# Optimization experiments

Measured on AMD Instinct MI355X. Metric: run time of the kernel, lower is better.

## Reference

```python
import jax, jax.numpy as jnp
import numpy as np

N_NODES = 200000
N_EDGES = 3200000
NUM_GRAPHS = 100
WIN = 30
H1, H2, OUT = 500, 20, 4


def setup_inputs() -> dict:
    key = jax.random.key(0)
    ks = jax.random.split(key, 8)
    features = jax.random.normal(ks[0], (N_NODES, WIN), dtype=jnp.float32)
    src = jax.random.randint(ks[1], (N_EDGES,), 0, N_NODES, dtype=jnp.int32)
    dst = jax.random.randint(ks[2], (N_EDGES,), 0, N_NODES, dtype=jnp.int32)
    # contiguous equal-size graphs: 2000 nodes per graph -> ids sorted 0..99
    graph_ids = (jnp.arange(N_NODES, dtype=jnp.int32) // (N_NODES // NUM_GRAPHS))
    W1 = jax.random.normal(ks[3], (WIN, H1), dtype=jnp.float32) / np.sqrt(WIN)
    b1 = jnp.zeros((H1,), jnp.float32)
    W2 = jax.random.normal(ks[4], (H1, H2), dtype=jnp.float32) / np.sqrt(H1)
    b2 = jnp.zeros((H2,), jnp.float32)
    W3 = jax.random.normal(ks[5], (H2, OUT), dtype=jnp.float32) / np.sqrt(H2)
    b3 = jnp.zeros((OUT,), jnp.float32)
    return {"features": features, "src": src, "dst": dst, "graph_ids": graph_ids,
            "num_graphs": NUM_GRAPHS, "W1": W1, "b1": b1, "W2": W2, "b2": b2,
            "W3": W3, "b3": b3}


def reference(features, src, dst, graph_ids, num_graphs, W1, b1, W2, b2, W3, b3):
    N = features.shape[0]
    ones = jnp.ones(src.shape[0], dtype=features.dtype)
    # DGL GraphConv norm='both': D_out^{-1/2} on src side, D_in^{-1/2} on dst side
    deg_out = jnp.maximum(jax.ops.segment_sum(ones, src, num_segments=N), 1.0)
    deg_in = jnp.maximum(jax.ops.segment_sum(ones, dst, num_segments=N), 1.0)
    x = features * jax.lax.rsqrt(deg_out)[:, None]
    # aggregate first (in_feats < out_feats), then dense transform
    agg = jax.ops.segment_sum(x[src], dst, num_segments=N)          # [N, 30]
    agg = agg * jax.lax.rsqrt(deg_in)[:, None]
    h = jax.nn.silu(agg @ W1 + b1)                                   # [N, 500]
    pooled = jax.ops.segment_max(h, graph_ids, num_segments=num_graphs)  # [G, 500]
    y = jax.nn.silu(pooled @ W2 + b2)                                # dropout = identity (eval)
    return jax.nn.sigmoid(y @ W3 + b3)                               # [G, 4]
```

## Files before the change

kernel.cpp:

```cpp
#include <hip/hip_runtime.h>
#include <hip/hip_fp16.h>

#define WIN 30
#define H1 500
#define H1P 512
#define H2 20
#define OUTD 4
#define CS 4
#define NBIN 49152
#define NBINW (NBIN/4)
#define NCH 48
#define RPB 512
#define MAXPB 9216
#define BINCHUNK 8192
#define NBMAX 400

typedef _Float16 f16x8 __attribute__((ext_vector_type(8)));
typedef float f32x4 __attribute__((ext_vector_type(4)));

__global__ __launch_bounds__(512) void k_hist(const int* __restrict__ src,
                                              unsigned* __restrict__ partial,
                                              int E) {
    __shared__ unsigned h[NBINW];
    const int tid = threadIdx.x;
    const int r = blockIdx.x / NCH, c = blockIdx.x % NCH;
    const int base = r * NBIN;
    for (int j = tid; j < NBINW; j += 512) h[j] = 0;
    __syncthreads();
    const int ce = ((E + NCH - 1) / NCH + 3) & ~3;
    const int start = c * ce;
    const int end = min(E, start + ce);
    for (int i = start + tid * 4; i < end; i += 512 * 4) {
        if (i + 3 < end) {
            int4 s4 = *(const int4*)(src + i);
            unsigned d;
            d = (unsigned)(s4.x - base); if (d < NBIN) atomicAdd(&h[d >> 2], 1u << ((d & 3) * 8));
            d = (unsigned)(s4.y - base); if (d < NBIN) atomicAdd(&h[d >> 2], 1u << ((d & 3) * 8));
            d = (unsigned)(s4.z - base); if (d < NBIN) atomicAdd(&h[d >> 2], 1u << ((d & 3) * 8));
            d = (unsigned)(s4.w - base); if (d < NBIN) atomicAdd(&h[d >> 2], 1u << ((d & 3) * 8));
        } else {
            for (int k = i; k < end; ++k) {
                unsigned d = (unsigned)(src[k] - base);
                if (d < NBIN) atomicAdd(&h[d >> 2], 1u << ((d & 3) * 8));
            }
        }
    }
    __syncthreads();
    unsigned* outp = partial + (size_t)blockIdx.x * NBINW;
    for (int j = tid; j < NBINW; j += 512) outp[j] = h[j];
}

__global__ __launch_bounds__(256) void k_merge(const unsigned* __restrict__ partial,
                                               int* __restrict__ degO, int N, int nr) {
    int w = blockIdx.x * 256 + threadIdx.x;
    if (w >= nr * NBINW) return;
    int r = w / NBINW, lw = w - r * NBINW;
    const unsigned* p = partial + (size_t)(r * NCH) * NBINW + lw;
    unsigned b0 = 0, b1 = 0, b2 = 0, b3 = 0;
    for (int c = 0; c < NCH; ++c) {
        unsigned v = p[(size_t)c * NBINW];
        b0 += v & 0xFFu; b1 += (v >> 8) & 0xFFu;
        b2 += (v >> 16) & 0xFFu; b3 += v >> 24;
    }
    int n0 = r * NBIN + 4 * lw;
    if (n0 + 3 < N) {
        *(int4*)(degO + n0) = make_int4((int)b0, (int)b1, (int)b2, (int)b3);
    } else if (n0 < N) {
        degO[n0] = (int)b0;
        if (n0 + 1 < N) degO[n0 + 1] = (int)b1;
        if (n0 + 2 < N) degO[n0 + 2] = (int)b2;
    }
}

__global__ __launch_bounds__(256) void k_prep(const float* __restrict__ feat,
                                              const int* __restrict__ degO,
                                              __half* __restrict__ xh, int N32) {
    int i = blockIdx.x * 256 + threadIdx.x;
    if (i < N32) {
        int n = i >> 5, d = i & 31;
        float v = 0.f;
        if (d < WIN) v = feat[(size_t)n * WIN + d] * rsqrtf((float)max(degO[n], 1));
        xh[i] = __float2half(v);
    }
}

__global__ __launch_bounds__(256) void k_w1prep(const float* __restrict__ W1,
                                                __half* __restrict__ w1cm) {
    int i = blockIdx.x * 256 + threadIdx.x;
    int c = i >> 5, k = i & 31;
    float v = (k < WIN && c < H1) ? W1[k * H1 + c] : 0.f;
    w1cm[i] = __float2half(v);
}

__global__ __launch_bounds__(1024) void k_bin(const int* __restrict__ src,
                                              const int* __restrict__ dst,
                                              int* __restrict__ gcur,
                                              unsigned* __restrict__ ebuf,
                                              int E, int NB) {
    __shared__ int cnt[NBMAX];
    __shared__ int base[NBMAX];
    const int tid = threadIdx.x;
    for (int j = tid; j < NB; j += 1024) cnt[j] = 0;
    __syncthreads();
    const int start = blockIdx.x * BINCHUNK;
    const int end = min(E, start + BINCHUNK);
    for (int i = start + tid; i < end; i += 1024)
        atomicAdd(&cnt[dst[i] >> 9], 1);
    __syncthreads();
    for (int j = tid; j < NB; j += 1024) {
        int c = cnt[j];
        base[j] = j * MAXPB + (c ? atomicAdd(&gcur[j], c) : 0);
        cnt[j] = 0;
    }
    __syncthreads();
    for (int i = start + tid; i < end; i += 1024) {
        int d = dst[i];
        int b = d >> 9;
        int idx = atomicAdd(&cnt[b], 1);
        int pos = base[b] + idx;
        if (pos < (b + 1) * MAXPB)
            ebuf[pos] = ((unsigned)src[i] << 9) | (unsigned)(d & 511);
    }
}

__global__ __launch_bounds__(1024) void k_agg(const __half* __restrict__ xh,
                                              const unsigned* __restrict__ ebuf,
                                              const int* __restrict__ gcur,
                                              __half* __restrict__ agg, int N) {
    __shared__ unsigned es[MAXPB];
    __shared__ int cnt[RPB + 1];
    __shared__ int cur[RPB];
    const int tid = threadIdx.x;
    const int b = blockIdx.x;
    for (int j = tid; j < RPB; j += 1024) { cnt[j + 1] = 0; cur[j] = 0; }
    if (tid == 0) cnt[0] = 0;
    __syncthreads();
    const int ne = min(gcur[b], MAXPB);
    const unsigned* eb = ebuf + (size_t)b * MAXPB;
    for (int i = tid; i < ne; i += 1024)
        atomicAdd(&cnt[(int)(eb[i] & (RPB - 1)) + 1], 1);
    __syncthreads();
    if (tid < 64) {
        const int i0 = tid * 8;
        int s[8];
        int run = 0;
#pragma unroll
        for (int k = 0; k < 8; ++k) { run += cnt[i0 + k + 1]; s[k] = run; }
        int inc = run;
#pragma unroll
        for (int o = 1; o < 64; o <<= 1) {
            int u = __shfl_up(inc, o, 64);
            if (tid >= o) inc += u;
        }
        const int ex = inc - run;
#pragma unroll
        for (int k = 0; k < 8; ++k) cnt[i0 + k + 1] = ex + s[k];
    }
    __syncthreads();
    for (int i = tid; i < ne; i += 1024) {
        unsigned p = eb[i];
        int ld = (int)(p & (RPB - 1));
        int idx = atomicAdd(&cur[ld], 1);
        es[cnt[ld] + idx] = p;
    }
    __syncthreads();
    for (int task = tid; task < RPB * 4; task += 1024) {
        const int node_l = task >> 2;
        const int c8 = (task & 3) * 8;
        const int o0 = cnt[node_l], o1 = cnt[node_l + 1];
        float a0 = 0.f, a1 = 0.f, a2 = 0.f, a3 = 0.f;
        float a4 = 0.f, a5 = 0.f, a6 = 0.f, a7 = 0.f;
        int j = o0;
#pragma unroll 2
        for (; j + 1 < o1; j += 2) {
            unsigned p0 = es[j], p1 = es[j + 1];
            union { uint4 u4; __half2 h2[4]; } x0, x1;
            x0.u4 = *(const uint4*)(xh + (size_t)(p0 >> 9) * 32 + c8);
            x1.u4 = *(const uint4*)(xh + (size_t)(p1 >> 9) * 32 + c8);
            a0 += __low2float(x0.h2[0]) + __low2float(x1.h2[0]);
            a1 += __high2float(x0.h2[0]) + __high2float(x1.h2[0]);
            a2 += __low2float(x0.h2[1]) + __low2float(x1.h2[1]);
            a3 += __high2float(x0.h2[1]) + __high2float(x1.h2[1]);
            a4 += __low2float(x0.h2[2]) + __low2float(x1.h2[2]);
            a5 += __high2float(x0.h2[2]) + __high2float(x1.h2[2]);
            a6 += __low2float(x0.h2[3]) + __low2float(x1.h2[3]);
            a7 += __high2float(x0.h2[3]) + __high2float(x1.h2[3]);
        }
        if (j < o1) {
            unsigned p0 = es[j];
            union { uint4 u4; __half2 h2[4]; } x0;
            x0.u4 = *(const uint4*)(xh + (size_t)(p0 >> 9) * 32 + c8);
            a0 += __low2float(x0.h2[0]);  a1 += __high2float(x0.h2[0]);
            a2 += __low2float(x0.h2[1]);  a3 += __high2float(x0.h2[1]);
            a4 += __low2float(x0.h2[2]);  a5 += __high2float(x0.h2[2]);
            a6 += __low2float(x0.h2[3]);  a7 += __high2float(x0.h2[3]);
        }
        const int node = b * RPB + node_l;
        if (node < N) {
            float deg = (float)(o1 - o0);
            float r = rsqrtf(fmaxf(deg, 1.f));
            union { uint4 u4; __half2 h2[4]; } y;
            y.h2[0] = __floats2half2_rn(a0 * r, a1 * r);
            y.h2[1] = __floats2half2_rn(a2 * r, a3 * r);
            y.h2[2] = __floats2half2_rn(a4 * r, a5 * r);
            y.h2[3] = __floats2half2_rn(a6 * r, a7 * r);
            *(uint4*)(agg + (size_t)node * 32 + c8) = y.u4;
        }
    }
}

__global__ __launch_bounds__(256) void k_gemm(const __half* __restrict__ agg,
                                              const __half* __restrict__ w1cm,
                                              const float* __restrict__ b1,
                                              float* __restrict__ pooled,
                                              int NPG, int G) {
    const int bid = blockIdx.x;
    const int g = bid / CS, c = bid % CS;
    const int tid = threadIdx.x;
    const int w = tid >> 6;
    const int l = tid & 63;
    const int lo = l & 15, hi = l >> 4;

    f16x8 bfr[8];
#pragma unroll
    for (int ct = 0; ct < 8; ++ct) {
        int col = c * 128 + ct * 16 + lo;
        bfr[ct] = *(const f16x8*)(w1cm + (size_t)col * 32 + hi * 8);
    }
    float vmax[8], vmin[8];
#pragma unroll
    for (int ct = 0; ct < 8; ++ct) { vmax[ct] = -INFINITY; vmin[ct] = INFINITY; }

    const int mts = NPG >> 4;
    for (int mt = w; mt < mts; mt += 4) {
        int node = g * NPG + mt * 16 + lo;
        f16x8 a = *(const f16x8*)(agg + (size_t)node * 32 + hi * 8);
#pragma unroll
        for (int ct = 0; ct < 8; ++ct) {
            f32x4 acc = {0.f, 0.f, 0.f, 0.f};
            acc = __builtin_amdgcn_mfma_f32_16x16x32_f16(a, bfr[ct], acc, 0, 0, 0);
#pragma unroll
            for (int q = 0; q < 4; ++q) {
                vmax[ct] = fmaxf(vmax[ct], acc[q]);
                vmin[ct] = fminf(vmin[ct], acc[q]);
            }
        }
    }
#pragma unroll
    for (int ct = 0; ct < 8; ++ct) {
        vmax[ct] = fmaxf(vmax[ct], __shfl_xor(vmax[ct], 16, 64));
        vmax[ct] = fmaxf(vmax[ct], __shfl_xor(vmax[ct], 32, 64));
        vmin[ct] = fminf(vmin[ct], __shfl_xor(vmin[ct], 16, 64));
        vmin[ct] = fminf(vmin[ct], __shfl_xor(vmin[ct], 32, 64));
    }
    __shared__ float red[2][4][8][16];
    if (hi == 0) {
#pragma unroll
        for (int ct = 0; ct < 8; ++ct) {
            red[0][w][ct][lo] = vmax[ct];
            red[1][w][ct][lo] = vmin[ct];
        }
    }
    __syncthreads();
    if (tid < 128) {
        int ct = tid >> 4, col16 = tid & 15;
        float m = fmaxf(fmaxf(red[0][0][ct][col16], red[0][1][ct][col16]),
                        fmaxf(red[0][2][ct][col16], red[0][3][ct][col16]));
        float n = fminf(fminf(red[1][0][ct][col16], red[1][1][ct][col16]),
                        fminf(red[1][2][ct][col16], red[1][3][ct][col16]));
        int col = c * 128 + ct * 16 + col16;
        float bb = (col < H1) ? b1[col] : 0.f;
        m += bb; n += bb;
        float sm = m / (1.f + __expf(-m));
        float sn = n / (1.f + __expf(-n));
        pooled[(size_t)g * H1P + col] = fmaxf(sm, sn);
    }
}

__global__ __launch_bounds__(64) void k_head(const float* __restrict__ pooled,
                                             const float* __restrict__ W2,
                                             const float* __restrict__ b2,
                                             const float* __restrict__ W3,
                                             const float* __restrict__ b3,
                                             float* __restrict__ out, int G) {
    const int g = blockIdx.x;
    const int t = threadIdx.x;
    __shared__ float y[H2];
    if (t < H2) {
        float acc = b2[t];
        for (int k = 0; k < H1; ++k)
            acc = fmaf(pooled[(size_t)g * H1P + k], W2[k * H2 + t], acc);
        y[t] = acc / (1.f + __expf(-acc));
    }
    __syncthreads();
    if (t < OUTD) {
        float acc = b3[t];
#pragma unroll
        for (int k = 0; k < H2; ++k) acc = fmaf(y[k], W3[k * OUTD + t], acc);
        out[g * OUTD + t] = 1.f / (1.f + __expf(-acc));
    }
}

static inline size_t align256(size_t x) { return (x + 255) & ~(size_t)255; }

extern "C" void kernel_launch(void* const* d_in, const int* in_sizes, int n_in,
                              void* d_out, int out_size, void* d_ws, size_t ws_size,
                              hipStream_t stream) {
    const float* feat = (const float*)d_in[0];
    const int*   src  = (const int*)d_in[1];
    const int*   dst  = (const int*)d_in[2];
    const float* W1 = (const float*)d_in[5];
    const float* b1 = (const float*)d_in[6];
    const float* W2 = (const float*)d_in[7];
    const float* b2 = (const float*)d_in[8];
    const float* W3 = (const float*)d_in[9];
    const float* b3 = (const float*)d_in[10];
    float* out = (float*)d_out;

    const int N = in_sizes[0] / WIN;
    const int E = in_sizes[1];
    const int G = out_size / OUTD;
    const int NPG = N / G;
    const int nr = (N + NBIN - 1) / NBIN;
    const int NB = (N + RPB - 1) / RPB;

    char* ws = (char*)d_ws;
    size_t off = 0;
    int*      degO    = (int*)(ws + off);      off += align256((size_t)N * 4);
    unsigned* partial = (unsigned*)(ws + off); off += align256((size_t)nr * NCH * NBINW * 4);
    __half*   xh      = (__half*)(ws + off);   off += align256((size_t)N * 32 * 2);
    __half*   w1cm    = (__half*)(ws + off);   off += align256((size_t)H1P * 32 * 2);
    float*    pooled  = (float*)(ws + off);    off += align256((size_t)G * H1P * 4);
    __half*   agg     = (__half*)(ws + off);   off += align256((size_t)N * 32 * 2);
    int*      gcur    = (int*)(ws + off);      off += align256((size_t)NB * 4);
    unsigned* ebuf    = (unsigned*)(ws + off); off += align256((size_t)NB * MAXPB * 4 + 256);
    (void)ws_size; (void)n_in;

    hipMemsetAsync(gcur, 0, (size_t)NB * 4, stream);

    k_hist<<<nr * NCH, 512, 0, stream>>>(src, partial, E);
    k_merge<<<(nr * NBINW + 255) / 256, 256, 0, stream>>>(partial, degO, N, nr);
    k_w1prep<<<(H1P * 32) / 256, 256, 0, stream>>>(W1, w1cm);
    k_prep<<<(N * 32 + 255) / 256, 256, 0, stream>>>(feat, degO, xh, N * 32);

    k_bin<<<(E + BINCHUNK - 1) / BINCHUNK, 1024, 0, stream>>>(src, dst, gcur, ebuf, E, NB);
    k_agg<<<NB, 1024, 0, stream>>>(xh, ebuf, gcur, agg, N);

    k_gemm<<<G * CS, 256, 0, stream>>>(agg, w1cm, b1, pooled, NPG, G);
    k_head<<<G, 64, 0, stream>>>(pooled, W2, b2, W3, b3, out, G);
}
```

Before: 165.8 us.

## Fuse aggregation with W1 MFMA and per-block min/max pooling

The aggregation kernel now keeps each block's aggregated rows in shared memory and runs the W1 MFMA on them directly. It reduces per-column max/min into shared memory through order-preserving uint atomics, then writes per-block partial results. A new kernel merges the partials per graph, applies bias, SiLU and the head, so the agg round trip through global memory and the separate GEMM launch go away. Block size is halved (256 rows, 512 threads) to fit shared memory and raise block count, at the cost of shared atomics and at most two graph slots per block.

```diff
diff --git a/kernel.cpp b/kernel.cpp
--- a/kernel.cpp
+++ b/kernel.cpp
@@ -6,17 +6,25 @@
 #define H1P 512
 #define H2 20
 #define OUTD 4
-#define CS 4
 #define NBIN 49152
 #define NBINW (NBIN/4)
 #define NCH 48
-#define RPB 512
-#define MAXPB 9216
+#define RPB 256
+#define MAXPB 4608
 #define BINCHUNK 8192
-#define NBMAX 400
+#define NBMAX 800
 
 typedef _Float16 f16x8 __attribute__((ext_vector_type(8)));
 typedef float f32x4 __attribute__((ext_vector_type(4)));
+
+__device__ __forceinline__ unsigned enc_f32(float f) {
+    unsigned b = __float_as_uint(f);
+    return b ^ ((unsigned)((int)b >> 31) | 0x80000000u);
+}
+__device__ __forceinline__ float dec_f32(unsigned u) {
+    unsigned b = (u & 0x80000000u) ? (u ^ 0x80000000u) : ~u;
+    return __uint_as_float(b);
+}
 
 __global__ __launch_bounds__(512) void k_hist(const int* __restrict__ src,
                                               unsigned* __restrict__ partial,
@@ -105,7 +113,7 @@
     const int start = blockIdx.x * BINCHUNK;
     const int end = min(E, start + BINCHUNK);
     for (int i = start + tid; i < end; i += 1024)
-        atomicAdd(&cnt[dst[i] >> 9], 1);
+        atomicAdd(&cnt[dst[i] >> 8], 1);
     __syncthreads();
     for (int j = tid; j < NB; j += 1024) {
         int c = cnt[j];
@@ -115,37 +123,45 @@
     __syncthreads();
     for (int i = start + tid; i < end; i += 1024) {
         int d = dst[i];
-        int b = d >> 9;
+        int b = d >> 8;
         int idx = atomicAdd(&cnt[b], 1);
         int pos = base[b] + idx;
         if (pos < (b + 1) * MAXPB)
-            ebuf[pos] = ((unsigned)src[i] << 9) | (unsigned)(d & 511);
-    }
-}
-
-__global__ __launch_bounds__(1024) void k_agg(const __half* __restrict__ xh,
-                                              const unsigned* __restrict__ ebuf,
-                                              const int* __restrict__ gcur,
-                                              __half* __restrict__ agg, int N) {
+            ebuf[pos] = ((unsigned)src[i] << 8) | (unsigned)(d & 255);
+    }
+}
+
+__global__ __launch_bounds__(512) void k_agg(const __half* __restrict__ xh,
+                                             const unsigned* __restrict__ ebuf,
+                                             const int* __restrict__ gcur,
+                                             const __half* __restrict__ w1cm,
+                                             unsigned* __restrict__ bmm,
+                                             int N, int NPG) {
     __shared__ unsigned es[MAXPB];
     __shared__ int cnt[RPB + 1];
     __shared__ int cur[RPB];
+    __shared__ __half xtile[RPB * 40];
+    __shared__ unsigned mmenc[2 * H1P * 2];
     const int tid = threadIdx.x;
     const int b = blockIdx.x;
-    for (int j = tid; j < RPB; j += 1024) { cnt[j + 1] = 0; cur[j] = 0; }
+    for (int j = tid; j < RPB; j += 512) { cnt[j + 1] = 0; cur[j] = 0; }
     if (tid == 0) cnt[0] = 0;
+    for (int j = tid; j < H1P * 2; j += 512) {
+        mmenc[2 * j + 0] = 0u;
+        mmenc[2 * j + 1] = 0xFFFFFFFFu;
+    }
     __syncthreads();
     const int ne = min(gcur[b], MAXPB);
     const unsigned* eb = ebuf + (size_t)b * MAXPB;
-    for (int i = tid; i < ne; i += 1024)
+    for (int i = tid; i < ne; i += 512)
         atomicAdd(&cnt[(int)(eb[i] & (RPB - 1)) + 1], 1);
     __syncthreads();
     if (tid < 64) {
-        const int i0 = tid * 8;
-        int s[8];
+        const int i0 = tid * 4;
+        int s[4];
         int run = 0;
 #pragma unroll
-        for (int k = 0; k < 8; ++k) { run += cnt[i0 + k + 1]; s[k] = run; }
+        for (int k = 0; k < 4; ++k) { run += cnt[i0 + k + 1]; s[k] = run; }
         int inc = run;
 #pragma unroll
         for (int o = 1; o < 64; o <<= 1) {
@@ -154,17 +170,17 @@
         }
         const int ex = inc - run;
 #pragma unroll
-        for (int k = 0; k < 8; ++k) cnt[i0 + k + 1] = ex + s[k];
-    }
-    __syncthreads();
-    for (int i = tid; i < ne; i += 1024) {
+        for (int k = 0; k < 4; ++k) cnt[i0 + k + 1] = ex + s[k];
+    }
+    __syncthreads();
+    for (int i = tid; i < ne; i += 512) {
         unsigned p = eb[i];
         int ld = (int)(p & (RPB - 1));
         int idx = atomicAdd(&cur[ld], 1);
         es[cnt[ld] + idx] = p;
     }
     __syncthreads();
-    for (int task = tid; task < RPB * 4; task += 1024) {
+    for (int task = tid; task < RPB * 4; task += 512) {
         const int node_l = task >> 2;
         const int c8 = (task & 3) * 8;
         const int o0 = cnt[node_l], o1 = cnt[node_l + 1];
@@ -175,8 +191,8 @@
         for (; j + 1 < o1; j += 2) {
             unsigned p0 = es[j], p1 = es[j + 1];
             union { uint4 u4; __half2 h2[4]; } x0, x1;
-            x0.u4 = *(const uint4*)(xh + (size_t)(p0 >> 9) * 32 + c8);
-            x1.u4 = *(const uint4*)(xh + (size_t)(p1 >> 9) * 32 + c8);
+            x0.u4 = *(const uint4*)(xh + (size_t)(p0 >> 8) * 32 + c8);
+            x1.u4 = *(const uint4*)(xh + (size_t)(p1 >> 8) * 32 + c8);
             a0 += __low2float(x0.h2[0]) + __low2float(x1.h2[0]);
             a1 += __high2float(x0.h2[0]) + __high2float(x1.h2[0]);
             a2 += __low2float(x0.h2[1]) + __low2float(x1.h2[1]);
@@ -189,107 +205,95 @@
         if (j < o1) {
             unsigned p0 = es[j];
             union { uint4 u4; __half2 h2[4]; } x0;
-            x0.u4 = *(const uint4*)(xh + (size_t)(p0 >> 9) * 32 + c8);
+            x0.u4 = *(const uint4*)(xh + (size_t)(p0 >> 8) * 32 + c8);
             a0 += __low2float(x0.h2[0]);  a1 += __high2float(x0.h2[0]);
             a2 += __low2float(x0.h2[1]);  a3 += __high2float(x0.h2[1]);
             a4 += __low2float(x0.h2[2]);  a5 += __high2float(x0.h2[2]);
             a6 += __low2float(x0.h2[3]);  a7 += __high2float(x0.h2[3]);
         }
-        const int node = b * RPB + node_l;
-        if (node < N) {
-            float deg = (float)(o1 - o0);
-            float r = rsqrtf(fmaxf(deg, 1.f));
-            union { uint4 u4; __half2 h2[4]; } y;
-            y.h2[0] = __floats2half2_rn(a0 * r, a1 * r);
-            y.h2[1] = __floats2half2_rn(a2 * r, a3 * r);
-            y.h2[2] = __floats2half2_rn(a4 * r, a5 * r);
-            y.h2[3] = __floats2half2_rn(a6 * r, a7 * r);
-            *(uint4*)(agg + (size_t)node * 32 + c8) = y.u4;
-        }
-    }
-}
-
-__global__ __launch_bounds__(256) void k_gemm(const __half* __restrict__ agg,
-                                              const __half* __restrict__ w1cm,
-                                              const float* __restrict__ b1,
-                                              float* __restrict__ pooled,
-                                              int NPG, int G) {
-    const int bid = blockIdx.x;
-    const int g = bid / CS, c = bid % CS;
-    const int tid = threadIdx.x;
-    const int w = tid >> 6;
-    const int l = tid & 63;
-    const int lo = l & 15, hi = l >> 4;
-
-    f16x8 bfr[8];
-#pragma unroll
-    for (int ct = 0; ct < 8; ++ct) {
-        int col = c * 128 + ct * 16 + lo;
-        bfr[ct] = *(const f16x8*)(w1cm + (size_t)col * 32 + hi * 8);
-    }
-    float vmax[8], vmin[8];
-#pragma unroll
-    for (int ct = 0; ct < 8; ++ct) { vmax[ct] = -INFINITY; vmin[ct] = INFINITY; }
-
-    const int mts = NPG >> 4;
-    for (int mt = w; mt < mts; mt += 4) {
-        int node = g * NPG + mt * 16 + lo;
-        f16x8 a = *(const f16x8*)(agg + (size_t)node * 32 + hi * 8);
-#pragma unroll
-        for (int ct = 0; ct < 8; ++ct) {
-            f32x4 acc = {0.f, 0.f, 0.f, 0.f};
-            acc = __builtin_amdgcn_mfma_f32_16x16x32_f16(a, bfr[ct], acc, 0, 0, 0);
-#pragma unroll
-            for (int q = 0; q < 4; ++q) {
-                vmax[ct] = fmaxf(vmax[ct], acc[q]);
-                vmin[ct] = fminf(vmin[ct], acc[q]);
+        float deg = (float)(o1 - o0);
+        float r = rsqrtf(fmaxf(deg, 1.f));
+        union { uint4 u4; __half2 h2[4]; } y;
+        y.h2[0] = __floats2half2_rn(a0 * r, a1 * r);
+        y.h2[1] = __floats2half2_rn(a2 * r, a3 * r);
+        y.h2[2] = __floats2half2_rn(a4 * r, a5 * r);
+        y.h2[3] = __floats2half2_rn(a6 * r, a7 * r);
+        *(uint4*)(&xtile[node_l * 40 + c8]) = y.u4;
+    }
+    __syncthreads();
+    {
+        const int wv = tid >> 6;
+        const int l = tid & 63;
+        const int lo = l & 15, hi = l >> 4;
+        const int bbase = b * RPB;
+        const int g0 = bbase / NPG;
+        f16x8 bfr[4];
+#pragma unroll
+        for (int j = 0; j < 4; ++j) {
+            int col = (wv * 4 + j) * 16 + lo;
+            bfr[j] = *(const f16x8*)(w1cm + (size_t)col * 32 + hi * 8);
+        }
+        for (int mt = 0; mt < RPB / 16; ++mt) {
+            if (bbase + mt * 16 >= N) break;
+            f16x8 a = *(const f16x8*)(&xtile[(mt * 16 + lo) * 40 + hi * 8]);
+            int slot = (bbase + mt * 16) / NPG - g0;
+#pragma unroll
+            for (int j = 0; j < 4; ++j) {
+                f32x4 acc = {0.f, 0.f, 0.f, 0.f};
+                acc = __builtin_amdgcn_mfma_f32_16x16x32_f16(a, bfr[j], acc, 0, 0, 0);
+                float mx = fmaxf(fmaxf(acc[0], acc[1]), fmaxf(acc[2], acc[3]));
+                float mn = fminf(fminf(acc[0], acc[1]), fminf(acc[2], acc[3]));
+                mx = fmaxf(mx, __shfl_xor(mx, 16, 64));
+                mx = fmaxf(mx, __shfl_xor(mx, 32, 64));
+                mn = fminf(mn, __shfl_xor(mn, 16, 64));
+                mn = fminf(mn, __shfl_xor(mn, 32, 64));
+                if (hi == 0) {
+                    int col = (wv * 4 + j) * 16 + lo;
+                    atomicMax(&mmenc[(slot * H1P + col) * 2 + 0], enc_f32(mx));
+                    atomicMin(&mmenc[(slot * H1P + col) * 2 + 1], enc_f32(mn));
+                }
             }
         }
     }
-#pragma unroll
-    for (int ct = 0; ct < 8; ++ct) {
-        vmax[ct] = fmaxf(vmax[ct], __shfl_xor(vmax[ct], 16, 64));
-        vmax[ct] = fmaxf(vmax[ct], __shfl_xor(vmax[ct], 32, 64));
-        vmin[ct] = fminf(vmin[ct], __shfl_xor(vmin[ct], 16, 64));
-        vmin[ct] = fminf(vmin[ct], __shfl_xor(vmin[ct], 32, 64));
-    }
-    __shared__ float red[2][4][8][16];
-    if (hi == 0) {
-#pragma unroll
-        for (int ct = 0; ct < 8; ++ct) {
-            red[0][w][ct][lo] = vmax[ct];
-            red[1][w][ct][lo] = vmin[ct];
-        }
-    }
-    __syncthreads();
-    if (tid < 128) {
-        int ct = tid >> 4, col16 = tid & 15;
-        float m = fmaxf(fmaxf(red[0][0][ct][col16], red[0][1][ct][col16]),
-                        fmaxf(red[0][2][ct][col16], red[0][3][ct][col16]));
-        float n = fminf(fminf(red[1][0][ct][col16], red[1][1][ct][col16]),
-                        fminf(red[1][2][ct][col16], red[1][3][ct][col16]));
-        int col = c * 128 + ct * 16 + col16;
-        float bb = (col < H1) ? b1[col] : 0.f;
-        m += bb; n += bb;
-        float sm = m / (1.f + __expf(-m));
-        float sn = n / (1.f + __expf(-n));
-        pooled[(size_t)g * H1P + col] = fmaxf(sm, sn);
-    }
-}
-
-__global__ __launch_bounds__(64) void k_head(const float* __restrict__ pooled,
-                                             const float* __restrict__ W2,
-                                             const float* __restrict__ b2,
-                                             const float* __restrict__ W3,
-                                             const float* __restrict__ b3,
-                                             float* __restrict__ out, int G) {
+    __syncthreads();
+    for (int j = tid; j < 2 * H1P * 2; j += 512)
+        bmm[(size_t)b * (2 * H1P * 2) + j] = mmenc[j];
+}
+
+__global__ __launch_bounds__(512) void k_rh(const unsigned* __restrict__ bmm,
+                                            const float* __restrict__ b1,
+                                            const float* __restrict__ W2,
+                                            const float* __restrict__ b2,
+                                            const float* __restrict__ W3,
+                                            const float* __restrict__ b3,
+                                            float* __restrict__ out,
+                                            int NPG, int NB) {
     const int g = blockIdx.x;
     const int t = threadIdx.x;
+    __shared__ float ph[H1P];
     __shared__ float y[H2];
+    unsigned me = 0u, mn = 0xFFFFFFFFu;
+    const int bFirst = (g * NPG) / RPB;
+    const int bLast = (g * NPG + NPG - 1) / RPB;
+    for (int b = bFirst; b <= bLast; ++b) {
+        int slot = g - (b * RPB) / NPG;
+        if (slot >= 0 && slot < 2) {
+            const unsigned* p = bmm + (size_t)b * (2 * H1P * 2) + ((size_t)slot * H1P + t) * 2;
+            me = max(me, p[0]);
+            mn = min(mn, p[1]);
+        }
+    }
+    float m = dec_f32(me), n = dec_f32(mn);
+    float bb = (t < H1) ? b1[t] : 0.f;
+    m += bb; n += bb;
+    float sm = m / (1.f + __expf(-m));
+    float sn = n / (1.f + __expf(-n));
+    ph[t] = fmaxf(sm, sn);
+    __syncthreads();
     if (t < H2) {
         float acc = b2[t];
         for (int k = 0; k < H1; ++k)
-            acc = fmaf(pooled[(size_t)g * H1P + k], W2[k * H2 + t], acc);
+            acc = fmaf(ph[k], W2[k * H2 + t], acc);
         y[t] = acc / (1.f + __expf(-acc));
     }
     __syncthreads();
@@ -330,10 +334,9 @@
     unsigned* partial = (unsigned*)(ws + off); off += align256((size_t)nr * NCH * NBINW * 4);
     __half*   xh      = (__half*)(ws + off);   off += align256((size_t)N * 32 * 2);
     __half*   w1cm    = (__half*)(ws + off);   off += align256((size_t)H1P * 32 * 2);
-    float*    pooled  = (float*)(ws + off);    off += align256((size_t)G * H1P * 4);
-    __half*   agg     = (__half*)(ws + off);   off += align256((size_t)N * 32 * 2);
     int*      gcur    = (int*)(ws + off);      off += align256((size_t)NB * 4);
     unsigned* ebuf    = (unsigned*)(ws + off); off += align256((size_t)NB * MAXPB * 4 + 256);
+    unsigned* bmm     = (unsigned*)(ws + off); off += align256((size_t)NB * 2 * H1P * 2 * 4);
     (void)ws_size; (void)n_in;
 
     hipMemsetAsync(gcur, 0, (size_t)NB * 4, stream);
@@ -344,8 +347,7 @@
     k_prep<<<(N * 32 + 255) / 256, 256, 0, stream>>>(feat, degO, xh, N * 32);
 
     k_bin<<<(E + BINCHUNK - 1) / BINCHUNK, 1024, 0, stream>>>(src, dst, gcur, ebuf, E, NB);
-    k_agg<<<NB, 1024, 0, stream>>>(xh, ebuf, gcur, agg, N);
-
-    k_gemm<<<G * CS, 256, 0, stream>>>(agg, w1cm, b1, pooled, NPG, G);
-    k_head<<<G, 64, 0, stream>>>(pooled, W2, b2, W3, b3, out, G);
-}
+    k_agg<<<NB, 512, 0, stream>>>(xh, ebuf, gcur, w1cm, bmm, N, NPG);
+
+    k_rh<<<G, 512, 0, stream>>>(bmm, b1, W2, b2, W3, b3, out, NPG, NB);
+}
```

Result: slower. 181.0 us (+9.2%).

## Fuse prep kernels, merge GEMM with head, drop memset, widen agg unroll

Applied to the files above, without the earlier changes.

Folds the degree merge, feature scaling and W1 conversion into one prep kernel. Fuses the per-graph GEMM/max-pool with the MLP head into one 512-thread block per graph. The gcur memset moves into the histogram kernel, and NBIN grows so nr drops from 5 to 4. The aggregation loop is unrolled by four. Together these cut launch count and intermediate traffic, but the fused GEMM now runs only 100 blocks with no split across column chunks, so parallelism drops.

```diff
diff --git a/kernel.cpp b/kernel.cpp
--- a/kernel.cpp
+++ b/kernel.cpp
@@ -6,8 +6,7 @@
 #define H1P 512
 #define H2 20
 #define OUTD 4
-#define CS 4
-#define NBIN 49152
+#define NBIN 61440
 #define NBINW (NBIN/4)
 #define NCH 48
 #define RPB 512
@@ -20,9 +19,12 @@
 
 __global__ __launch_bounds__(512) void k_hist(const int* __restrict__ src,
                                               unsigned* __restrict__ partial,
-                                              int E) {
+                                              int* __restrict__ gcur,
+                                              int E, int NB) {
     __shared__ unsigned h[NBINW];
     const int tid = threadIdx.x;
+    if (blockIdx.x == 0)
+        for (int j = tid; j < NB; j += 512) gcur[j] = 0;
     const int r = blockIdx.x / NCH, c = blockIdx.x % NCH;
     const int base = r * NBIN;
     for (int j = tid; j < NBINW; j += 512) h[j] = 0;
@@ -50,46 +52,60 @@
     for (int j = tid; j < NBINW; j += 512) outp[j] = h[j];
 }
 
-__global__ __launch_bounds__(256) void k_merge(const unsigned* __restrict__ partial,
-                                               int* __restrict__ degO, int N, int nr) {
-    int w = blockIdx.x * 256 + threadIdx.x;
-    if (w >= nr * NBINW) return;
-    int r = w / NBINW, lw = w - r * NBINW;
-    const unsigned* p = partial + (size_t)(r * NCH) * NBINW + lw;
-    unsigned b0 = 0, b1 = 0, b2 = 0, b3 = 0;
-    for (int c = 0; c < NCH; ++c) {
-        unsigned v = p[(size_t)c * NBINW];
-        b0 += v & 0xFFu; b1 += (v >> 8) & 0xFFu;
-        b2 += (v >> 16) & 0xFFu; b3 += v >> 24;
-    }
-    int n0 = r * NBIN + 4 * lw;
-    if (n0 + 3 < N) {
-        *(int4*)(degO + n0) = make_int4((int)b0, (int)b1, (int)b2, (int)b3);
-    } else if (n0 < N) {
-        degO[n0] = (int)b0;
-        if (n0 + 1 < N) degO[n0 + 1] = (int)b1;
-        if (n0 + 2 < N) degO[n0 + 2] = (int)b2;
-    }
-}
-
-__global__ __launch_bounds__(256) void k_prep(const float* __restrict__ feat,
-                                              const int* __restrict__ degO,
-                                              __half* __restrict__ xh, int N32) {
-    int i = blockIdx.x * 256 + threadIdx.x;
-    if (i < N32) {
-        int n = i >> 5, d = i & 31;
-        float v = 0.f;
-        if (d < WIN) v = feat[(size_t)n * WIN + d] * rsqrtf((float)max(degO[n], 1));
-        xh[i] = __float2half(v);
-    }
-}
-
-__global__ __launch_bounds__(256) void k_w1prep(const float* __restrict__ W1,
-                                                __half* __restrict__ w1cm) {
-    int i = blockIdx.x * 256 + threadIdx.x;
-    int c = i >> 5, k = i & 31;
-    float v = (k < WIN && c < H1) ? W1[k * H1 + c] : 0.f;
-    w1cm[i] = __float2half(v);
+__global__ __launch_bounds__(256) void k_prep2(const unsigned* __restrict__ partial,
+                                               const float* __restrict__ feat,
+                                               const float* __restrict__ W1,
+                                               __half* __restrict__ xh,
+                                               __half* __restrict__ w1cm,
+                                               int N, int nmb) {
+    const int tid = threadIdx.x;
+    if (blockIdx.x == nmb) {
+        for (int i = tid; i < H1P * 32; i += 256) {
+            int c = i >> 5, k = i & 31;
+            float v = (k < WIN && c < H1) ? W1[k * H1 + c] : 0.f;
+            w1cm[i] = __float2half(v);
+        }
+        return;
+    }
+    __shared__ float rs[1024];
+    {
+        int w = blockIdx.x * 256 + tid;
+        int node0 = 4 * w;
+        int r = node0 / NBIN;
+        int lw = (node0 - r * NBIN) >> 2;
+        const unsigned* p = partial + (size_t)(r * NCH) * NBINW + lw;
+        unsigned b0 = 0, b1 = 0, b2 = 0, b3 = 0;
+        for (int c = 0; c < NCH; ++c) {
+            unsigned v = p[(size_t)c * NBINW];
+            b0 += v & 0xFFu; b1 += (v >> 8) & 0xFFu;
+            b2 += (v >> 16) & 0xFFu; b3 += v >> 24;
+        }
+        rs[tid * 4 + 0] = rsqrtf((float)max((int)b0, 1));
+        rs[tid * 4 + 1] = rsqrtf((float)max((int)b1, 1));
+        rs[tid * 4 + 2] = rsqrtf((float)max((int)b2, 1));
+        rs[tid * 4 + 3] = rsqrtf((float)max((int)b3, 1));
+    }
+    __syncthreads();
+    const int nbase = blockIdx.x * 1024;
+    for (int task = tid; task < 1024 * 4; task += 256) {
+        int node_l = task >> 2;
+        int node = nbase + node_l;
+        if (node >= N) break;
+        int c8 = (task & 3) * 8;
+        float r = rs[node_l];
+        float f[8];
+#pragma unroll
+        for (int q = 0; q < 8; ++q) {
+            int d = c8 + q;
+            f[q] = (d < WIN) ? feat[(size_t)node * WIN + d] * r : 0.f;
+        }
+        union { uint4 u4; __half2 h2[4]; } y;
+        y.h2[0] = __floats2half2_rn(f[0], f[1]);
+        y.h2[1] = __floats2half2_rn(f[2], f[3]);
+        y.h2[2] = __floats2half2_rn(f[4], f[5]);
+        y.h2[3] = __floats2half2_rn(f[6], f[7]);
+        *(uint4*)(xh + (size_t)node * 32 + c8) = y.u4;
+    }
 }
 
 __global__ __launch_bounds__(1024) void k_bin(const int* __restrict__ src,
@@ -171,22 +187,23 @@
         float a0 = 0.f, a1 = 0.f, a2 = 0.f, a3 = 0.f;
         float a4 = 0.f, a5 = 0.f, a6 = 0.f, a7 = 0.f;
         int j = o0;
-#pragma unroll 2
-        for (; j + 1 < o1; j += 2) {
-            unsigned p0 = es[j], p1 = es[j + 1];
-            union { uint4 u4; __half2 h2[4]; } x0, x1;
+        for (; j + 3 < o1; j += 4) {
+            unsigned p0 = es[j], p1 = es[j + 1], p2 = es[j + 2], p3 = es[j + 3];
+            union { uint4 u4; __half2 h2[4]; } x0, x1, x2, x3;
             x0.u4 = *(const uint4*)(xh + (size_t)(p0 >> 9) * 32 + c8);
             x1.u4 = *(const uint4*)(xh + (size_t)(p1 >> 9) * 32 + c8);
-            a0 += __low2float(x0.h2[0]) + __low2float(x1.h2[0]);
-            a1 += __high2float(x0.h2[0]) + __high2float(x1.h2[0]);
-            a2 += __low2float(x0.h2[1]) + __low2float(x1.h2[1]);
-            a3 += __high2float(x0.h2[1]) + __high2float(x1.h2[1]);
-            a4 += __low2float(x0.h2[2]) + __low2float(x1.h2[2]);
-            a5 += __high2float(x0.h2[2]) + __high2float(x1.h2[2]);
-            a6 += __low2float(x0.h2[3]) + __low2float(x1.h2[3]);
-            a7 += __high2float(x0.h2[3]) + __high2float(x1.h2[3]);
-        }
-        if (j < o1) {
+            x2.u4 = *(const uint4*)(xh + (size_t)(p2 >> 9) * 32 + c8);
+            x3.u4 = *(const uint4*)(xh + (size_t)(p3 >> 9) * 32 + c8);
+            a0 += __low2float(x0.h2[0]) + __low2float(x1.h2[0]) + __low2float(x2.h2[0]) + __low2float(x3.h2[0]);
+            a1 += __high2float(x0.h2[0]) + __high2float(x1.h2[0]) + __high2float(x2.h2[0]) + __high2float(x3.h2[0]);
+            a2 += __low2float(x0.h2[1]) + __low2float(x1.h2[1]) + __low2float(x2.h2[1]) + __low2float(x3.h2[1]);
+            a3 += __high2float(x0.h2[1]) + __high2float(x1.h2[1]) + __high2float(x2.h2[1]) + __high2float(x3.h2[1]);
+            a4 += __low2float(x0.h2[2]) + __low2float(x1.h2[2]) + __low2float(x2.h2[2]) + __low2float(x3.h2[2]);
+            a5 += __high2float(x0.h2[2]) + __high2float(x1.h2[2]) + __high2float(x2.h2[2]) + __high2float(x3.h2[2]);
+            a6 += __low2float(x0.h2[3]) + __low2float(x1.h2[3]) + __low2float(x2.h2[3]) + __low2float(x3.h2[3]);
+            a7 += __high2float(x0.h2[3]) + __high2float(x1.h2[3]) + __high2float(x2.h2[3]) + __high2float(x3.h2[3]);
+        }
+        for (; j < o1; ++j) {
             unsigned p0 = es[j];
             union { uint4 u4; __half2 h2[4]; } x0;
             x0.u4 = *(const uint4*)(xh + (size_t)(p0 >> 9) * 32 + c8);
@@ -209,95 +226,83 @@
     }
 }
 
-__global__ __launch_bounds__(256) void k_gemm(const __half* __restrict__ agg,
-                                              const __half* __restrict__ w1cm,
-                                              const float* __restrict__ b1,
-                                              float* __restrict__ pooled,
-                                              int NPG, int G) {
-    const int bid = blockIdx.x;
-    const int g = bid / CS, c = bid % CS;
-    const int tid = threadIdx.x;
-    const int w = tid >> 6;
+__global__ __launch_bounds__(512) void k_gh(const __half* __restrict__ agg,
+                                            const __half* __restrict__ w1cm,
+                                            const float* __restrict__ b1,
+                                            const float* __restrict__ W2,
+                                            const float* __restrict__ b2,
+                                            const float* __restrict__ W3,
+                                            const float* __restrict__ b3,
+                                            float* __restrict__ out,
+                                            int NPG, int N) {
+    const int g = blockIdx.x;
+    const int tid = threadIdx.x;
+    const int wv = tid >> 6;
     const int l = tid & 63;
     const int lo = l & 15, hi = l >> 4;
-
-    f16x8 bfr[8];
-#pragma unroll
-    for (int ct = 0; ct < 8; ++ct) {
-        int col = c * 128 + ct * 16 + lo;
-        bfr[ct] = *(const f16x8*)(w1cm + (size_t)col * 32 + hi * 8);
-    }
-    float vmax[8], vmin[8];
-#pragma unroll
-    for (int ct = 0; ct < 8; ++ct) { vmax[ct] = -INFINITY; vmin[ct] = INFINITY; }
+    __shared__ float lmax[H1P];
+    __shared__ float lmin[H1P];
+    __shared__ float ph[H1P];
+    __shared__ float y[H2];
+
+    f16x8 bfr[4];
+#pragma unroll
+    for (int j = 0; j < 4; ++j) {
+        int col = wv * 64 + j * 16 + lo;
+        bfr[j] = *(const f16x8*)(w1cm + (size_t)col * 32 + hi * 8);
+    }
+    float vmax[4], vmin[4];
+#pragma unroll
+    for (int j = 0; j < 4; ++j) { vmax[j] = -INFINITY; vmin[j] = INFINITY; }
 
     const int mts = NPG >> 4;
-    for (int mt = w; mt < mts; mt += 4) {
+    for (int mt = 0; mt < mts; ++mt) {
         int node = g * NPG + mt * 16 + lo;
         f16x8 a = *(const f16x8*)(agg + (size_t)node * 32 + hi * 8);
 #pragma unroll
-        for (int ct = 0; ct < 8; ++ct) {
+        for (int j = 0; j < 4; ++j) {
             f32x4 acc = {0.f, 0.f, 0.f, 0.f};
-            acc = __builtin_amdgcn_mfma_f32_16x16x32_f16(a, bfr[ct], acc, 0, 0, 0);
-#pragma unroll
-            for (int q = 0; q < 4; ++q) {
-                vmax[ct] = fmaxf(vmax[ct], acc[q]);
-                vmin[ct] = fminf(vmin[ct], acc[q]);
-            }
-        }
-    }
-#pragma unroll
-    for (int ct = 0; ct < 8; ++ct) {
-        vmax[ct] = fmaxf(vmax[ct], __shfl_xor(vmax[ct], 16, 64));
-        vmax[ct] = fmaxf(vmax[ct], __shfl_xor(vmax[ct], 32, 64));
-        vmin[ct] = fminf(vmin[ct], __shfl_xor(vmin[ct], 16, 64));
-        vmin[ct] = fminf(vmin[ct], __shfl_xor(vmin[ct], 32, 64));
-    }
-    __shared__ float red[2][4][8][16];
-    if (hi == 0) {
-#pragma unroll
-        for (int ct = 0; ct < 8; ++ct) {
-            red[0][w][ct][lo] = vmax[ct];
-            red[1][w][ct][lo] = vmin[ct];
-        }
-    }
-    __syncthreads();
-    if (tid < 128) {
-        int ct = tid >> 4, col16 = tid & 15;
-        float m = fmaxf(fmaxf(red[0][0][ct][col16], red[0][1][ct][col16]),
-                        fmaxf(red[0][2][ct][col16], red[0][3][ct][col16]));
-        float n = fminf(fminf(red[1][0][ct][col16], red[1][1][ct][col16]),
-                        fminf(red[1][2][ct][col16], red[1][3][ct][col16]));
-        int col = c * 128 + ct * 16 + col16;
-        float bb = (col < H1) ? b1[col] : 0.f;
-        m += bb; n += bb;
+            acc = __builtin_amdgcn_mfma_f32_16x16x32_f16(a, bfr[j], acc, 0, 0, 0);
+            float mx = fmaxf(fmaxf(acc[0], acc[1]), fmaxf(acc[2], acc[3]));
+            float mn = fminf(fminf(acc[0], acc[1]), fminf(acc[2], acc[3]));
+            vmax[j] = fmaxf(vmax[j], mx);
+            vmin[j] = fminf(vmin[j], mn);
+        }
+    }
+#pragma unroll
+    for (int j = 0; j < 4; ++j) {
+        vmax[j] = fmaxf(vmax[j], __shfl_xor(vmax[j], 16, 64));
+        vmax[j] = fmaxf(vmax[j], __shfl_xor(vmax[j], 32, 64));
+        vmin[j] = fminf(vmin[j], __shfl_xor(vmin[j], 16, 64));
+        vmin[j] = fminf(vmin[j], __shfl_xor(vmin[j], 32, 64));
+        if (hi == 0) {
+            int col = wv * 64 + j * 16 + lo;
+            lmax[col] = vmax[j];
+            lmin[col] = vmin[j];
+        }
+    }
+    __syncthreads();
+    {
+        int t = tid;
+        float bb = (t < H1) ? b1[t] : 0.f;
+        float m = lmax[t] + bb, n = lmin[t] + bb;
         float sm = m / (1.f + __expf(-m));
         float sn = n / (1.f + __expf(-n));
-        pooled[(size_t)g * H1P + col] = fmaxf(sm, sn);
-    }
-}
-
-__global__ __launch_bounds__(64) void k_head(const float* __restrict__ pooled,
-                                             const float* __restrict__ W2,
-                                             const float* __restrict__ b2,
-                                             const float* __restrict__ W3,
-                                             const float* __restrict__ b3,
-                                             float* __restrict__ out, int G) {
-    const int g = blockIdx.x;
-    const int t = threadIdx.x;
-    __shared__ float y[H2];
-    if (t < H2) {
-        float acc = b2[t];
+        ph[t] = fmaxf(sm, sn);
+    }
+    __syncthreads();
+    if (tid < H2) {
+        float acc = b2[tid];
         for (int k = 0; k < H1; ++k)
-            acc = fmaf(pooled[(size_t)g * H1P + k], W2[k * H2 + t], acc);
-        y[t] = acc / (1.f + __expf(-acc));
-    }
-    __syncthreads();
-    if (t < OUTD) {
-        float acc = b3[t];
-#pragma unroll
-        for (int k = 0; k < H2; ++k) acc = fmaf(y[k], W3[k * OUTD + t], acc);
-        out[g * OUTD + t] = 1.f / (1.f + __expf(-acc));
+            acc = fmaf(ph[k], W2[k * H2 + tid], acc);
+        y[tid] = acc / (1.f + __expf(-acc));
+    }
+    __syncthreads();
+    if (tid < OUTD) {
+        float acc = b3[tid];
+#pragma unroll
+        for (int k = 0; k < H2; ++k) acc = fmaf(y[k], W3[k * OUTD + tid], acc);
+        out[g * OUTD + tid] = 1.f / (1.f + __expf(-acc));
     }
 }
 
@@ -323,29 +328,21 @@
     const int NPG = N / G;
     const int nr = (N + NBIN - 1) / NBIN;
     const int NB = (N + RPB - 1) / RPB;
+    const int nmb = (N + 1023) / 1024;
 
     char* ws = (char*)d_ws;
     size_t off = 0;
-    int*      degO    = (int*)(ws + off);      off += align256((size_t)N * 4);
     unsigned* partial = (unsigned*)(ws + off); off += align256((size_t)nr * NCH * NBINW * 4);
     __half*   xh      = (__half*)(ws + off);   off += align256((size_t)N * 32 * 2);
     __half*   w1cm    = (__half*)(ws + off);   off += align256((size_t)H1P * 32 * 2);
-    float*    pooled  = (float*)(ws + off);    off += align256((size_t)G * H1P * 4);
     __half*   agg     = (__half*)(ws + off);   off += align256((size_t)N * 32 * 2);
     int*      gcur    = (int*)(ws + off);      off += align256((size_t)NB * 4);
     unsigned* ebuf    = (unsigned*)(ws + off); off += align256((size_t)NB * MAXPB * 4 + 256);
     (void)ws_size; (void)n_in;
 
-    hipMemsetAsync(gcur, 0, (size_t)NB * 4, stream);
-
-    k_hist<<<nr * NCH, 512, 0, stream>>>(src, partial, E);
-    k_merge<<<(nr * NBINW + 255) / 256, 256, 0, stream>>>(partial, degO, N, nr);
-    k_w1prep<<<(H1P * 32) / 256, 256, 0, stream>>>(W1, w1cm);
-    k_prep<<<(N * 32 + 255) / 256, 256, 0, stream>>>(feat, degO, xh, N * 32);
-
+    k_hist<<<nr * NCH, 512, 0, stream>>>(src, partial, gcur, E, NB);
+    k_prep2<<<nmb + 1, 256, 0, stream>>>(partial, feat, W1, xh, w1cm, N, nmb);
     k_bin<<<(E + BINCHUNK - 1) / BINCHUNK, 1024, 0, stream>>>(src, dst, gcur, ebuf, E, NB);
     k_agg<<<NB, 1024, 0, stream>>>(xh, ebuf, gcur, agg, N);
-
-    k_gemm<<<G * CS, 256, 0, stream>>>(agg, w1cm, b1, pooled, NPG, G);
-    k_head<<<G, 64, 0, stream>>>(pooled, W2, b2, W3, b3, out, G);
-}
+    k_gh<<<G, 512, 0, stream>>>(agg, w1cm, b1, W2, b2, W3, b3, out, NPG, N);
+}
```

Result: slower. 190.5 us (+14.9%).
